# Optimization experiments

Measured on AMD Instinct MI355X. Metric: run time of the kernel, lower is better.

The kernel has to match this reference:

```python
import jax, jax.numpy as jnp
import numpy as np

H = 64          # hidden_dim
I = 4           # input_dim
L = 4           # num_layers
O = 5           # output_dim
B = 256         # batch
T = 2048        # seq_len


def setup_inputs() -> dict:
    key = jax.random.key(0)
    ks = jax.random.split(key, 20)
    s = 1.0 / np.sqrt(H)  # PyTorch GRU init scale
    x = jax.random.normal(ks[0], (B, T, I), dtype=jnp.float32)
    # layer 0 input->hidden weights ([3H, I]); layers 1..3 input is H
    w_ih0 = jax.random.uniform(ks[1], (3 * H, I), jnp.float32, -s, s)
    w_ih_rest = jax.random.uniform(ks[2], (L - 1, 3 * H, H), jnp.float32, -s, s)
    w_hh = jax.random.uniform(ks[3], (L, 3 * H, H), jnp.float32, -s, s)
    b_ih = jax.random.uniform(ks[4], (L, 3 * H), jnp.float32, -s, s)
    b_hh = jax.random.uniform(ks[5], (L, 3 * H), jnp.float32, -s, s)
    fc_w = jax.random.uniform(ks[6], (O, H), jnp.float32, -s, s)
    fc_b = jax.random.uniform(ks[7], (O,), jnp.float32, -s, s)
    return {"x": x, "w_ih0": w_ih0, "w_ih_rest": w_ih_rest, "w_hh": w_hh,
            "b_ih": b_ih, "b_hh": b_hh, "fc_w": fc_w, "fc_b": fc_b}


def _gru_layer(x_seq, w_ih, w_hh, b_ih, b_hh):
    """x_seq: [B,T,Din] -> [B,T,H]. PyTorch GRU cell equations."""
    # Precompute all input-side gate projections in one GEMM: [B,T,3H]
    gx = jnp.einsum('btd,gd->btg', x_seq, w_ih) + b_ih
    gx = jnp.swapaxes(gx, 0, 1)  # [T,B,3H] for scan over time

    def step(h, gx_t):
        gh = h @ w_hh.T + b_hh                 # [B,3H]
        xr, xz, xn = jnp.split(gx_t, 3, axis=-1)
        hr, hz, hn = jnp.split(gh, 3, axis=-1)
        r = jax.nn.sigmoid(xr + hr)
        z = jax.nn.sigmoid(xz + hz)
        n = jnp.tanh(xn + r * hn)
        h_new = (1.0 - z) * n + z * h
        return h_new, h_new

    h0 = jnp.zeros((x_seq.shape[0], H), dtype=x_seq.dtype)
    _, hs = jax.lax.scan(step, h0, gx)
    return jnp.swapaxes(hs, 0, 1)  # [B,T,H]


def reference(x, w_ih0, w_ih_rest, w_hh, b_ih, b_hh, fc_w, fc_b):
    # 4 stacked GRU layers (dropout=0.3 between layers is a no-op in eval mode)
    out = _gru_layer(x, w_ih0, w_hh[0], b_ih[0], b_hh[0])
    for l in range(1, L):
        out = _gru_layer(out, w_ih_rest[l - 1], w_hh[l], b_ih[l], b_hh[l])
    # final linear head on last timestep: [B,O]
    return out[:, -1, :] @ fc_w.T + fc_b
```

## Files before the change

### kernel.cpp

```cpp
#include <hip/hip_runtime.h>

#define T_LEN 2048
#define NTHREADS 896

__global__ __launch_bounds__(NTHREADS)
__attribute__((amdgpu_waves_per_eu(4, 4)))
void gru_fused(const float* __restrict__ x,
               const float* __restrict__ w_ih0,
               const float* __restrict__ w_ih_rest,
               const float* __restrict__ w_hh,
               const float* __restrict__ b_ih,
               const float* __restrict__ b_hh,
               const float* __restrict__ fc_w,
               const float* __restrict__ fc_b,
               float* __restrict__ out)
{
    __shared__ float smem[21504];
    float* xs   = smem;
    float* hst  = xs + 8192;
    float* gbuf = hst + 256;
    float* w0s  = gbuf + 1344;
    float* bihs = w0s + 768;
    float* bhhs = bihs + 768;

    const int tid = threadIdx.x;
    const int b   = blockIdx.x;

    {
        const float4* xg = (const float4*)(x + (size_t)b * (T_LEN * 4));
        float4* xd = (float4*)xs;
        for (int i = tid; i < T_LEN; i += NTHREADS) xd[i] = xg[i];
    }
    if (tid < 192)                ((float4*)w0s)[tid]        = ((const float4*)w_ih0)[tid];
    else if (tid < 384)           ((float4*)bihs)[tid - 192] = ((const float4*)b_ih)[tid - 192];
    else if (tid < 576)           ((float4*)bhhs)[tid - 384] = ((const float4*)b_hh)[tid - 384];
    if (tid < 256) hst[tid] = 0.0f;

    const int g2   = tid >> 7;
    const int r7_  = tid & 127;
    const int c    = r7_ >> 1;
    const int half = r7_ & 1;
    const int src  = (g2 < 3) ? g2 : (g2 - 3);

    float4 w4[3][8];
    {
        const float* wsrc = (g2 < 3) ? (w_ih_rest + g2 * (192 * 64))
                                     : (w_hh      + (g2 - 3) * (192 * 64));
        #pragma unroll
        for (int i = 0; i < 3; ++i) {
            const float4* p = (const float4*)(wsrc + (i * 64 + c) * 64 + half * 32);
            #pragma unroll
            for (int q = 0; q < 8; ++q) w4[i][q] = p[q];
        }
    }
    #pragma unroll
    for (int i = 0; i < 3; ++i)
        #pragma unroll
        for (int q = 0; q < 8; ++q)
            asm volatile("" : "+v"(w4[i][q].x), "+v"(w4[i][q].y),
                             "+v"(w4[i][q].z), "+v"(w4[i][q].w));

    const int cl = tid >> 6;
    const int cc = tid & 63;
    __syncthreads();

    const float4* vb4 = (const float4*)(hst + src * 64 + half * 32);

    for (int s = 0; s < T_LEN + 3; ++s) {
        float a0 = 0.f, a1 = 0.f, a2 = 0.f;
        #pragma unroll
        for (int q = 0; q < 8; ++q) {
            const float4 f = vb4[q];
            a0 = fmaf(f.x, w4[0][q].x, a0); a0 = fmaf(f.y, w4[0][q].y, a0);
            a0 = fmaf(f.z, w4[0][q].z, a0); a0 = fmaf(f.w, w4[0][q].w, a0);
            a1 = fmaf(f.x, w4[1][q].x, a1); a1 = fmaf(f.y, w4[1][q].y, a1);
            a1 = fmaf(f.z, w4[1][q].z, a1); a1 = fmaf(f.w, w4[1][q].w, a1);
            a2 = fmaf(f.x, w4[2][q].x, a2); a2 = fmaf(f.y, w4[2][q].y, a2);
            a2 = fmaf(f.z, w4[2][q].z, a2); a2 = fmaf(f.w, w4[2][q].w, a2);
        }
        a0 += __shfl_xor(a0, 1);
        a1 += __shfl_xor(a1, 1);
        a2 += __shfl_xor(a2, 1);
        if (half == 0) {
            gbuf[g2 * 192 +       c] = a0;
            gbuf[g2 * 192 +  64 + c] = a1;
            gbuf[g2 * 192 + 128 + c] = a2;
        }
        __syncthreads();

        if (tid < 256) {
            const int t = s - cl;
            if (t >= 0 && t < T_LEN) {
                float xr, xz, xn;
                if (cl == 0) {
                    const float4 xv = ((const float4*)xs)[t];
                    const float4 u0 = ((const float4*)w0s)[cc];
                    const float4 u1 = ((const float4*)w0s)[64 + cc];
                    const float4 u2 = ((const float4*)w0s)[128 + cc];
                    xr = bihs[cc]       + xv.x * u0.x + xv.y * u0.y + xv.z * u0.z + xv.w * u0.w;
                    xz = bihs[64 + cc]  + xv.x * u1.x + xv.y * u1.y + xv.z * u1.z + xv.w * u1.w;
                    xn = bihs[128 + cc] + xv.x * u2.x + xv.y * u2.y + xv.z * u2.z + xv.w * u2.w;
                } else {
                    xr = bihs[cl * 192 +       cc] + gbuf[(cl - 1) * 192 +       cc];
                    xz = bihs[cl * 192 +  64 + cc] + gbuf[(cl - 1) * 192 +  64 + cc];
                    xn = bihs[cl * 192 + 128 + cc] + gbuf[(cl - 1) * 192 + 128 + cc];
                }
                const float hr = bhhs[cl * 192 +       cc] + gbuf[(3 + cl) * 192 +       cc];
                const float hz = bhhs[cl * 192 +  64 + cc] + gbuf[(3 + cl) * 192 +  64 + cc];
                const float hn = bhhs[cl * 192 + 128 + cc] + gbuf[(3 + cl) * 192 + 128 + cc];
                const float hold = hst[cl * 64 + cc];

                const float r = 1.0f / (1.0f + __expf(-(xr + hr)));
                const float z = 1.0f / (1.0f + __expf(-(xz + hz)));
                const float e = __expf(2.0f * (xn + r * hn));
                const float n = 1.0f - 2.0f / (e + 1.0f);
                hst[cl * 64 + cc] = n + z * (hold - n);
            }
        }
        __syncthreads();
    }

    if (tid < 5) {
        float acc = fc_b[tid];
        const float* wf = fc_w + tid * 64;
        #pragma unroll
        for (int k = 0; k < 64; ++k) acc = fmaf(hst[3 * 64 + k], wf[k], acc);
        out[(size_t)b * 5 + tid] = acc;
    }
}

extern "C" void kernel_launch(void* const* d_in, const int* in_sizes, int n_in,
                              void* d_out, int out_size, void* d_ws, size_t ws_size,
                              hipStream_t stream) {
    const float* x         = (const float*)d_in[0];
    const float* w_ih0     = (const float*)d_in[1];
    const float* w_ih_rest = (const float*)d_in[2];
    const float* w_hh      = (const float*)d_in[3];
    const float* b_ih      = (const float*)d_in[4];
    const float* b_hh      = (const float*)d_in[5];
    const float* fc_w      = (const float*)d_in[6];
    const float* fc_b      = (const float*)d_in[7];

    gru_fused<<<dim3(256), dim3(NTHREADS), 0, stream>>>(
        x, w_ih0, w_ih_rest, w_hh, b_ih, b_hh, fc_w, fc_b, (float*)d_out);
}
```

Before: 2.021 ms.

## Chunk time into 16-step blocks and batch input projections across chunks

Replaces the per-timestep wavefront, where every step computed both input and recurrent matvecs for all layers with two barriers, with a chunked pipeline. Each layer's recurrent matvec keeps only W_hh in registers across 8 waves of 512 threads. Input-side projections for the next layer are computed a whole 16-step chunk at a time from a double-buffered shared history, spread across the chunk's iterations. This removes one barrier per step and takes the W_ih work off the serial critical path, at the cost of more complex chunk scheduling and global-memory reads of W_ih inside the loop.

Result: slower. 3.492 ms (+72.8%).

```diff
diff --git a/kernel.cpp b/kernel.cpp
--- a/kernel.cpp
+++ b/kernel.cpp
@@ -1,10 +1,11 @@
 #include <hip/hip_runtime.h>
 
-#define T_LEN 2048
-#define NTHREADS 896
+#define T_LEN    2048
+#define CHUNK    16
+#define NCHUNK   128
+#define NTHREADS 512
 
-__global__ __launch_bounds__(NTHREADS)
-__attribute__((amdgpu_waves_per_eu(4, 4)))
+__global__ __launch_bounds__(NTHREADS, 1)
 void gru_fused(const float* __restrict__ x,
                const float* __restrict__ w_ih0,
                const float* __restrict__ w_ih_rest,
@@ -15,116 +16,148 @@
                const float* __restrict__ fc_b,
                float* __restrict__ out)
 {
-    __shared__ float smem[21504];
-    float* xs   = smem;
-    float* hst  = xs + 8192;
-    float* gbuf = hst + 256;
-    float* w0s  = gbuf + 1344;
-    float* bihs = w0s + 768;
-    float* bhhs = bihs + 768;
+    __shared__ __align__(16) float hist[4][2][CHUNK][64];
+    __shared__ __align__(16) float gxb [4][2][CHUNK][192];
 
     const int tid = threadIdx.x;
     const int b   = blockIdx.x;
+    const int w   = tid >> 6;
+    const int c   = tid & 63;
 
+    const int l   = w >> 1;
+    const int sub = w & 1;
+    const int pr  = c >> 1;
+    const int hh  = c & 1;
+    const int gg  = sub * 32 + pr;
+
+    float4 wr[24];
     {
-        const float4* xg = (const float4*)(x + (size_t)b * (T_LEN * 4));
-        float4* xd = (float4*)xs;
-        for (int i = tid; i < T_LEN; i += NTHREADS) xd[i] = xg[i];
+        const float* base = w_hh + l * 12288;
+        #pragma unroll
+        for (int i = 0; i < 3; ++i)
+            #pragma unroll
+            for (int q = 0; q < 8; ++q)
+                wr[i * 8 + q] = *(const float4*)(base + (i * 64 + gg) * 64 + hh * 32 + q * 4);
     }
-    if (tid < 192)                ((float4*)w0s)[tid]        = ((const float4*)w_ih0)[tid];
-    else if (tid < 384)           ((float4*)bihs)[tid - 192] = ((const float4*)b_ih)[tid - 192];
-    else if (tid < 576)           ((float4*)bhhs)[tid - 384] = ((const float4*)b_hh)[tid - 384];
-    if (tid < 256) hst[tid] = 0.0f;
+    const float bhr = b_hh[l * 192 +       gg];
+    const float bhz = b_hh[l * 192 +  64 + gg];
+    const float bhn = b_hh[l * 192 + 128 + gg];
 
-    const int g2   = tid >> 7;
-    const int r7_  = tid & 127;
-    const int c    = r7_ >> 1;
-    const int half = r7_ & 1;
-    const int src  = (g2 < 3) ? g2 : (g2 - 3);
+    const int   fr   = 64 * w + c;
+    const int   lgw  = fr / 192 + 1;
+    const int   rG   = fr % 192;
+    const float biasG = b_ih[lgw * 192 + rG];
+    const float* wG   = w_ih_rest + (lgw - 1) * 12288 + rG * 64;
 
-    float4 w4[3][8];
-    {
-        const float* wsrc = (g2 < 3) ? (w_ih_rest + g2 * (192 * 64))
-                                     : (w_hh      + (g2 - 3) * (192 * 64));
-        #pragma unroll
-        for (int i = 0; i < 3; ++i) {
-            const float4* p = (const float4*)(wsrc + (i * 64 + c) * 64 + half * 32);
-            #pragma unroll
-            for (int q = 0; q < 8; ++q) w4[i][q] = p[q];
-        }
-    }
-    #pragma unroll
-    for (int i = 0; i < 3; ++i)
-        #pragma unroll
-        for (int q = 0; q < 8; ++q)
-            asm volatile("" : "+v"(w4[i][q].x), "+v"(w4[i][q].y),
-                             "+v"(w4[i][q].z), "+v"(w4[i][q].w));
+    const float* wG8   = w_ih_rest + 2 * 12288 + (128 + c) * 64 + w * 8;
+    const float biasG8 = b_ih[3 * 192 + 128 + c];
 
-    const int cl = tid >> 6;
-    const int cc = tid & 63;
+    const int  r0    = (w - 4) * 64 + c;
+    const bool hasL0 = (w >= 4 && w <= 6);
+    float4 w0v = make_float4(0.f, 0.f, 0.f, 0.f);
+    float  b0v = 0.f;
+    if (hasL0) { w0v = *(const float4*)(w_ih0 + r0 * 4); b0v = b_ih[r0]; }
+
+    const float* xrow = x + (size_t)b * (T_LEN * 4);
+
+    if (w < 4) hist[w][1][CHUNK - 1][c] = 0.f;
+    float hc = 0.f;
     __syncthreads();
 
-    const float4* vb4 = (const float4*)(hst + src * 64 + half * 32);
+    for (int p = -1; p <= 133; ++p) {
+        const int  kR    = p - 2 * l;            const bool rAct  = (0 <= kR  && kR  < NCHUNK);
+        const int  bufR  = kR & 1;
+        const int  cgO   = p - 2 * lgw + 1;      const bool gAct  = (0 <= cgO && cgO < NCHUNK);
+        const int  bufO  = cgO & 1;
+        const int  cg3   = p - 5;                const bool g8Act = (0 <= cg3 && cg3 < NCHUNK);
+        const int  buf3  = cg3 & 1;
+        const int  cg0   = p + 1;                const bool g0Act = hasL0 && (0 <= cg0 && cg0 < NCHUNK);
+        const int  buf0  = cg0 & 1;
 
-    for (int s = 0; s < T_LEN + 3; ++s) {
-        float a0 = 0.f, a1 = 0.f, a2 = 0.f;
-        #pragma unroll
-        for (int q = 0; q < 8; ++q) {
-            const float4 f = vb4[q];
-            a0 = fmaf(f.x, w4[0][q].x, a0); a0 = fmaf(f.y, w4[0][q].y, a0);
-            a0 = fmaf(f.z, w4[0][q].z, a0); a0 = fmaf(f.w, w4[0][q].w, a0);
-            a1 = fmaf(f.x, w4[1][q].x, a1); a1 = fmaf(f.y, w4[1][q].y, a1);
-            a1 = fmaf(f.z, w4[1][q].z, a1); a1 = fmaf(f.w, w4[1][q].w, a1);
-            a2 = fmaf(f.x, w4[2][q].x, a2); a2 = fmaf(f.y, w4[2][q].y, a2);
-            a2 = fmaf(f.z, w4[2][q].z, a2); a2 = fmaf(f.w, w4[2][q].w, a2);
+        #pragma unroll 1
+        for (int j = 0; j < CHUNK; ++j) {
+            if (rAct) {
+                const float* hv  = (j == 0) ? hist[l][bufR ^ 1][CHUNK - 1]
+                                            : hist[l][bufR][j - 1];
+                const float* hvh = hv + hh * 32;
+                float a0 = 0.f, a1 = 0.f, a2 = 0.f;
+                #pragma unroll
+                for (int q = 0; q < 8; ++q) {
+                    const float4 f = *(const float4*)(hvh + q * 4);
+                    a0 = fmaf(f.x, wr[     q].x, a0); a0 = fmaf(f.y, wr[     q].y, a0);
+                    a0 = fmaf(f.z, wr[     q].z, a0); a0 = fmaf(f.w, wr[     q].w, a0);
+                    a1 = fmaf(f.x, wr[ 8 + q].x, a1); a1 = fmaf(f.y, wr[ 8 + q].y, a1);
+                    a1 = fmaf(f.z, wr[ 8 + q].z, a1); a1 = fmaf(f.w, wr[ 8 + q].w, a1);
+                    a2 = fmaf(f.x, wr[16 + q].x, a2); a2 = fmaf(f.y, wr[16 + q].y, a2);
+                    a2 = fmaf(f.z, wr[16 + q].z, a2); a2 = fmaf(f.w, wr[16 + q].w, a2);
+                }
+                a0 += __shfl_xor(a0, 1);
+                a1 += __shfl_xor(a1, 1);
+                a2 += __shfl_xor(a2, 1);
+                if (hh == 0) {
+                    const float xr = gxb[l][bufR][j][      gg];
+                    const float xz = gxb[l][bufR][j][ 64 + gg];
+                    const float xn = gxb[l][bufR][j][128 + gg];
+                    const float rr = 1.f / (1.f + __expf(-(xr + (a0 + bhr))));
+                    const float zz = 1.f / (1.f + __expf(-(xz + (a1 + bhz))));
+                    const float e  = __expf(2.f * (xn + rr * (a2 + bhn)));
+                    const float nn = 1.f - 2.f / (e + 1.f);
+                    hc = nn + zz * (hc - nn);
+                    hist[l][bufR][j][gg] = hc;
+                }
+            }
+            if (gAct && (j & 1) == 0) {
+                const int s = j >> 1;
+                const float4 wa = *(const float4*)(wG + s * 8);
+                const float4 wb = *(const float4*)(wG + s * 8 + 4);
+                #pragma unroll
+                for (int t = 0; t < CHUNK; ++t) {
+                    const float* hsrc = hist[lgw - 1][bufO][t] + s * 8;
+                    const float4 ha = *(const float4*)(hsrc);
+                    const float4 hb = *(const float4*)(hsrc + 4);
+                    float d = ha.x * wa.x;
+                    d = fmaf(ha.y, wa.y, d); d = fmaf(ha.z, wa.z, d); d = fmaf(ha.w, wa.w, d);
+                    d = fmaf(hb.x, wb.x, d); d = fmaf(hb.y, wb.y, d);
+                    d = fmaf(hb.z, wb.z, d); d = fmaf(hb.w, wb.w, d);
+                    float* dst = &gxb[lgw][bufO][t][rG];
+                    *dst = (s == 0) ? (biasG + d) : (*dst + d);
+                }
+            }
+            if (g8Act && j == 2 * w + 1) {
+                const float4 wa = *(const float4*)(wG8);
+                const float4 wb = *(const float4*)(wG8 + 4);
+                #pragma unroll
+                for (int t = 0; t < CHUNK; ++t) {
+                    const float* hsrc = hist[2][buf3][t] + w * 8;
+                    const float4 ha = *(const float4*)(hsrc);
+                    const float4 hb = *(const float4*)(hsrc + 4);
+                    float d = ha.x * wa.x;
+                    d = fmaf(ha.y, wa.y, d); d = fmaf(ha.z, wa.z, d); d = fmaf(ha.w, wa.w, d);
+                    d = fmaf(hb.x, wb.x, d); d = fmaf(hb.y, wb.y, d);
+                    d = fmaf(hb.z, wb.z, d); d = fmaf(hb.w, wb.w, d);
+                    float* dst = &gxb[3][buf3][t][128 + c];
+                    *dst = (w == 0) ? (biasG8 + d) : (*dst + d);
+                }
+            }
+            if (g0Act && j == 3) {
+                #pragma unroll
+                for (int t = 0; t < CHUNK; ++t) {
+                    const float4 xv = *(const float4*)(xrow + (cg0 * CHUNK + t) * 4);
+                    float d = xv.x * w0v.x;
+                    d = fmaf(xv.y, w0v.y, d); d = fmaf(xv.z, w0v.z, d); d = fmaf(xv.w, w0v.w, d);
+                    gxb[0][buf0][t][r0] = b0v + d;
+                }
+            }
+            __syncthreads();
         }
-        a0 += __shfl_xor(a0, 1);
-        a1 += __shfl_xor(a1, 1);
-        a2 += __shfl_xor(a2, 1);
-        if (half == 0) {
-            gbuf[g2 * 192 +       c] = a0;
-            gbuf[g2 * 192 +  64 + c] = a1;
-            gbuf[g2 * 192 + 128 + c] = a2;
-        }
-        __syncthreads();
-
-        if (tid < 256) {
-            const int t = s - cl;
-            if (t >= 0 && t < T_LEN) {
-                float xr, xz, xn;
-                if (cl == 0) {
-                    const float4 xv = ((const float4*)xs)[t];
-                    const float4 u0 = ((const float4*)w0s)[cc];
-                    const float4 u1 = ((const float4*)w0s)[64 + cc];
-                    const float4 u2 = ((const float4*)w0s)[128 + cc];
-                    xr = bihs[cc]       + xv.x * u0.x + xv.y * u0.y + xv.z * u0.z + xv.w * u0.w;
-                    xz = bihs[64 + cc]  + xv.x * u1.x + xv.y * u1.y + xv.z * u1.z + xv.w * u1.w;
-                    xn = bihs[128 + cc] + xv.x * u2.x + xv.y * u2.y + xv.z * u2.z + xv.w * u2.w;
-                } else {
-                    xr = bihs[cl * 192 +       cc] + gbuf[(cl - 1) * 192 +       cc];
-                    xz = bihs[cl * 192 +  64 + cc] + gbuf[(cl - 1) * 192 +  64 + cc];
-                    xn = bihs[cl * 192 + 128 + cc] + gbuf[(cl - 1) * 192 + 128 + cc];
-                }
-                const float hr = bhhs[cl * 192 +       cc] + gbuf[(3 + cl) * 192 +       cc];
-                const float hz = bhhs[cl * 192 +  64 + cc] + gbuf[(3 + cl) * 192 +  64 + cc];
-                const float hn = bhhs[cl * 192 + 128 + cc] + gbuf[(3 + cl) * 192 + 128 + cc];
-                const float hold = hst[cl * 64 + cc];
-
-                const float r = 1.0f / (1.0f + __expf(-(xr + hr)));
-                const float z = 1.0f / (1.0f + __expf(-(xz + hz)));
-                const float e = __expf(2.0f * (xn + r * hn));
-                const float n = 1.0f - 2.0f / (e + 1.0f);
-                hst[cl * 64 + cc] = n + z * (hold - n);
-            }
-        }
-        __syncthreads();
     }
 
     if (tid < 5) {
         float acc = fc_b[tid];
         const float* wf = fc_w + tid * 64;
         #pragma unroll
-        for (int k = 0; k < 64; ++k) acc = fmaf(hst[3 * 64 + k], wf[k], acc);
+        for (int k2 = 0; k2 < 64; ++k2)
+            acc = fmaf(hist[3][1][CHUNK - 1][k2], wf[k2], acc);
         out[(size_t)b * 5 + tid] = acc;
     }
 }
```
